# Optimization experiments

Measured on AMD Instinct MI355X. Metric: run time of the kernel, lower is better.

Reference implementation:

```python
import jax, jax.numpy as jnp
import numpy as np


def setup_inputs() -> dict:
    key = jax.random.key(0)
    x = jax.random.normal(key, (1024, 65536), dtype=jnp.float32)
    return {"input": x}


def reference(input) -> jnp.ndarray:
    B = input.shape[0]
    flat = input.reshape(B, -1)            # [B, N]
    N = flat.shape[1]
    idx = int(N * 0.8)                      # 80th-percentile position (ascending sort)
    cutoff = jnp.sort(flat, axis=-1)[:, idx]  # [B]
    cutoff = jax.lax.stop_gradient(cutoff)
    # broadcast cutoff back over all non-batch dims
    cutoff = cutoff.reshape((B,) + (1,) * (input.ndim - 1))
    return jax.nn.relu(input - cutoff)
```

## Files before the change

kernel.cpp:

```cpp
#include <hip/hip_runtime.h>


#define TPB   512
#define F4PT  32
#define NB    2048
#define CAP   6144
#define TINY  64
#define BLO   0.72f
#define BHI   0.98f

__device__ __forceinline__ unsigned f2ord(float f) {
    unsigned u = __float_as_uint(f);
    return (u & 0x80000000u) ? ~u : (u | 0x80000000u);
}
__device__ __forceinline__ float ord2f(unsigned u) {
    unsigned b = (u & 0x80000000u) ? (u ^ 0x80000000u) : ~u;
    return __uint_as_float(b);
}

__device__ __forceinline__ void hist_select(const unsigned* hist, unsigned r, int tid,
                                            unsigned* wsum, unsigned* wbase,
                                            int* s_bin, unsigned* s_cum) {
    const int lane = tid & 63, wid = tid >> 6;
    const int b0 = tid * (NB / TPB);
    unsigned h0 = hist[b0], h1 = hist[b0+1], h2 = hist[b0+2], h3 = hist[b0+3];
    unsigned s = h0 + h1 + h2 + h3;
    unsigned incl = s;
    #pragma unroll
    for (int off = 1; off < 64; off <<= 1) {
        unsigned t = __shfl_up(incl, off);
        if (lane >= off) incl += t;
    }
    if (lane == 63) wsum[wid] = incl;
    __syncthreads();
    if (tid == 0) {
        unsigned c = 0;
        #pragma unroll
        for (int w = 0; w < TPB/64; ++w) { wbase[w] = c; c += wsum[w]; }
    }
    __syncthreads();
    unsigned excl = wbase[wid] + incl - s;
    if (r >= excl && r < excl + s) {
        unsigned c = excl;
        if (r < c + h0)        { *s_bin = b0;     *s_cum = c; }
        else { c += h0; if (r < c + h1) { *s_bin = b0 + 1; *s_cum = c; }
        else { c += h1; if (r < c + h2) { *s_bin = b0 + 2; *s_cum = c; }
        else { c += h2;                   *s_bin = b0 + 3; *s_cum = c; } } }
    }
    __syncthreads();
}

__global__ __launch_bounds__(TPB)
void xsrelu_fused(const float* __restrict__ in, float* __restrict__ out,
                  int N, int k) {
    const int row  = blockIdx.x;
    const int tid  = threadIdx.x;
    const int lane = tid & 63;
    const float SCALE = (float)NB / (BHI - BLO);
    const float4* __restrict__ rowv = (const float4*)(in + (size_t)row * (size_t)N);
    float4* __restrict__ outv = (float4*)(out + (size_t)row * (size_t)N);

    __shared__ unsigned hist[NB];
    __shared__ unsigned cand[CAP];
    __shared__ unsigned tiny[TINY];
    __shared__ unsigned wsum[TPB/64], wbase[TPB/64];
    __shared__ unsigned s_cnt, s_below, s_cum, s_tc;
    __shared__ int s_bin, s_fb;
    __shared__ float s_cut;

    for (int i = tid; i < NB; i += TPB) hist[i] = 0u;
    if (tid == 0) { s_cnt = 0u; s_below = 0u; s_tc = 0u; s_fb = 0; }
    __syncthreads();

    float4 v[F4PT];
    #pragma unroll
    for (int j = 0; j < F4PT; ++j) v[j] = rowv[tid + j * TPB];

    unsigned below = 0;
    #pragma unroll
    for (int j = 0; j < F4PT; ++j) {
        const float f0 = v[j].x, f1 = v[j].y, f2 = v[j].z, f3 = v[j].w;
        below += (f0 < BLO) ? 1u : 0u;
        below += (f1 < BLO) ? 1u : 0u;
        below += (f2 < BLO) ? 1u : 0u;
        below += (f3 < BLO) ? 1u : 0u;
        if (f0 >= BLO && f0 < BHI) { unsigned p = atomicAdd(&s_cnt, 1u); if (p < CAP) cand[p] = __float_as_uint(f0); }
        if (f1 >= BLO && f1 < BHI) { unsigned p = atomicAdd(&s_cnt, 1u); if (p < CAP) cand[p] = __float_as_uint(f1); }
        if (f2 >= BLO && f2 < BHI) { unsigned p = atomicAdd(&s_cnt, 1u); if (p < CAP) cand[p] = __float_as_uint(f2); }
        if (f3 >= BLO && f3 < BHI) { unsigned p = atomicAdd(&s_cnt, 1u); if (p < CAP) cand[p] = __float_as_uint(f3); }
    }
    #pragma unroll
    for (int o = 32; o > 0; o >>= 1) below += __shfl_down(below, o);
    if (lane == 0) atomicAdd(&s_below, below);
    __syncthreads();

    const unsigned M0 = s_cnt;
    const long long r2ll = (long long)k - (long long)s_below;
    const bool fast = (M0 <= CAP) && (r2ll >= 0) && (r2ll < (long long)M0);

    if (fast) {
        const unsigned r2 = (unsigned)r2ll;
        for (unsigned i = tid; i < M0; i += TPB) {
            float f = __uint_as_float(cand[i]);
            int b = (int)((f - BLO) * SCALE);
            b = b < 0 ? 0 : (b >= NB ? NB - 1 : b);
            atomicAdd(&hist[b], 1u);
        }
        __syncthreads();
        hist_select(hist, r2, tid, wsum, wbase, &s_bin, &s_cum);
        const int bin = s_bin;
        const unsigned r3 = r2 - s_cum;
        for (unsigned i = tid; i < M0; i += TPB) {
            unsigned u = cand[i];
            float f = __uint_as_float(u);
            int b = (int)((f - BLO) * SCALE);
            b = b < 0 ? 0 : (b >= NB ? NB - 1 : b);
            if (b == bin) { unsigned p = atomicAdd(&s_tc, 1u); if (p < TINY) tiny[p] = u; }
        }
        __syncthreads();
        const unsigned c = s_tc;
        if (c > TINY) { if (tid == 0) s_fb = 1; }
        else if (tid < 64) {
            unsigned uj = (lane < (int)c) ? tiny[lane] : 0xFFFFFFFFu;
            unsigned less = 0, eq = 0;
            for (unsigned i2 = 0; i2 < c; ++i2) {
                unsigned ui = tiny[i2];
                less += (ui < uj) ? 1u : 0u;
                eq   += (ui == uj) ? 1u : 0u;
            }
            bool cond = (lane < (int)c) && (less <= r3) && (r3 < less + eq);
            unsigned long long cm = __ballot(cond);
            if (cond && lane == __ffsll((long long)cm) - 1)
                s_cut = __uint_as_float(uj);
        }
    } else {
        if (tid == 0) s_fb = 1;
    }
    __syncthreads();

    if (s_fb) {
        unsigned prefix = 0;
        unsigned rr = (unsigned)k;
        const int shifts[3] = {21, 10, 0};
        const int bitsc[3]  = {11, 11, 10};
        for (int pass = 0; pass < 3; ++pass) {
            const int sh = shifts[pass];
            const unsigned nbm = (1u << bitsc[pass]) - 1u;
            for (int i = tid; i < NB; i += TPB) hist[i] = 0u;
            __syncthreads();
            #pragma unroll
            for (int j = 0; j < F4PT; ++j) {
                const float vals[4] = {v[j].x, v[j].y, v[j].z, v[j].w};
                #pragma unroll
                for (int q = 0; q < 4; ++q) {
                    unsigned u = f2ord(vals[q]);
                    if (pass == 0 || (u >> (sh + bitsc[pass])) == prefix)
                        atomicAdd(&hist[(u >> sh) & nbm], 1u);
                }
            }
            __syncthreads();
            hist_select(hist, rr, tid, wsum, wbase, &s_bin, &s_cum);
            prefix = (prefix << bitsc[pass]) | (unsigned)s_bin;
            rr -= s_cum;
        }
        if (tid == 0) s_cut = ord2f(prefix);
        __syncthreads();
    }

    const float cut = s_cut;

    #pragma unroll
    for (int j = 0; j < F4PT; ++j) {
        float4 o;
        o.x = fmaxf(v[j].x - cut, 0.0f);
        o.y = fmaxf(v[j].y - cut, 0.0f);
        o.z = fmaxf(v[j].z - cut, 0.0f);
        o.w = fmaxf(v[j].w - cut, 0.0f);
        outv[tid + j * TPB] = o;
    }
}

extern "C" void kernel_launch(void* const* d_in, const int* in_sizes, int n_in,
                              void* d_out, int out_size, void* d_ws, size_t ws_size,
                              hipStream_t stream) {
    const float* in = (const float*)d_in[0];
    float* out = (float*)d_out;
    const int N = 65536;
    const int B = in_sizes[0] / N;
    const int k = (int)(((long long)N * 4) / 5);

    xsrelu_fused<<<dim3(B), dim3(TPB), 0, stream>>>(in, out, N, k);
}
```

Measured before the change: 475.0 us.

## Stream row from global memory instead of holding it in registers

New measurement: 481.4 us. Within noise of the previous version (+1.3%).

```diff
diff --git a/kernel.cpp b/kernel.cpp
--- a/kernel.cpp
+++ b/kernel.cpp
@@ -1,13 +1,14 @@
 #include <hip/hip_runtime.h>
 
 
-#define TPB   512
-#define F4PT  32
+#define TPB   256
+#define BPT   8
 #define NB    2048
 #define CAP   6144
 #define TINY  64
 #define BLO   0.72f
 #define BHI   0.98f
+#define NWAVE (TPB/64)
 
 __device__ __forceinline__ unsigned f2ord(float f) {
     unsigned u = __float_as_uint(f);
@@ -17,14 +18,17 @@
     unsigned b = (u & 0x80000000u) ? (u ^ 0x80000000u) : ~u;
     return __uint_as_float(b);
 }
+__device__ __forceinline__ bool in_band(float f) { return f >= BLO && f < BHI; }
 
 __device__ __forceinline__ void hist_select(const unsigned* hist, unsigned r, int tid,
                                             unsigned* wsum, unsigned* wbase,
                                             int* s_bin, unsigned* s_cum) {
     const int lane = tid & 63, wid = tid >> 6;
-    const int b0 = tid * (NB / TPB);
-    unsigned h0 = hist[b0], h1 = hist[b0+1], h2 = hist[b0+2], h3 = hist[b0+3];
-    unsigned s = h0 + h1 + h2 + h3;
+    const int b0 = tid * BPT;
+    unsigned h[BPT];
+    unsigned s = 0;
+    #pragma unroll
+    for (int j = 0; j < BPT; ++j) { h[j] = hist[b0 + j]; s += h[j]; }
     unsigned incl = s;
     #pragma unroll
     for (int off = 1; off < 64; off <<= 1) {
@@ -36,16 +40,17 @@
     if (tid == 0) {
         unsigned c = 0;
         #pragma unroll
-        for (int w = 0; w < TPB/64; ++w) { wbase[w] = c; c += wsum[w]; }
+        for (int w = 0; w < NWAVE; ++w) { wbase[w] = c; c += wsum[w]; }
     }
     __syncthreads();
     unsigned excl = wbase[wid] + incl - s;
     if (r >= excl && r < excl + s) {
         unsigned c = excl;
-        if (r < c + h0)        { *s_bin = b0;     *s_cum = c; }
-        else { c += h0; if (r < c + h1) { *s_bin = b0 + 1; *s_cum = c; }
-        else { c += h1; if (r < c + h2) { *s_bin = b0 + 2; *s_cum = c; }
-        else { c += h2;                   *s_bin = b0 + 3; *s_cum = c; } } }
+        #pragma unroll
+        for (int j = 0; j < BPT; ++j) {
+            if (r < c + h[j]) { *s_bin = b0 + j; *s_cum = c; break; }
+            c += h[j];
+        }
     }
     __syncthreads();
 }
@@ -56,6 +61,7 @@
     const int row  = blockIdx.x;
     const int tid  = threadIdx.x;
     const int lane = tid & 63;
+    const int nv   = N >> 2;
     const float SCALE = (float)NB / (BHI - BLO);
     const float4* __restrict__ rowv = (const float4*)(in + (size_t)row * (size_t)N);
     float4* __restrict__ outv = (float4*)(out + (size_t)row * (size_t)N);
@@ -63,7 +69,7 @@
     __shared__ unsigned hist[NB];
     __shared__ unsigned cand[CAP];
     __shared__ unsigned tiny[TINY];
-    __shared__ unsigned wsum[TPB/64], wbase[TPB/64];
+    __shared__ unsigned wsum[NWAVE], wbase[NWAVE];
     __shared__ unsigned s_cnt, s_below, s_cum, s_tc;
     __shared__ int s_bin, s_fb;
     __shared__ float s_cut;
@@ -72,22 +78,18 @@
     if (tid == 0) { s_cnt = 0u; s_below = 0u; s_tc = 0u; s_fb = 0; }
     __syncthreads();
 
-    float4 v[F4PT];
-    #pragma unroll
-    for (int j = 0; j < F4PT; ++j) v[j] = rowv[tid + j * TPB];
-
     unsigned below = 0;
-    #pragma unroll
-    for (int j = 0; j < F4PT; ++j) {
-        const float f0 = v[j].x, f1 = v[j].y, f2 = v[j].z, f3 = v[j].w;
-        below += (f0 < BLO) ? 1u : 0u;
-        below += (f1 < BLO) ? 1u : 0u;
-        below += (f2 < BLO) ? 1u : 0u;
-        below += (f3 < BLO) ? 1u : 0u;
-        if (f0 >= BLO && f0 < BHI) { unsigned p = atomicAdd(&s_cnt, 1u); if (p < CAP) cand[p] = __float_as_uint(f0); }
-        if (f1 >= BLO && f1 < BHI) { unsigned p = atomicAdd(&s_cnt, 1u); if (p < CAP) cand[p] = __float_as_uint(f1); }
-        if (f2 >= BLO && f2 < BHI) { unsigned p = atomicAdd(&s_cnt, 1u); if (p < CAP) cand[p] = __float_as_uint(f2); }
-        if (f3 >= BLO && f3 < BHI) { unsigned p = atomicAdd(&s_cnt, 1u); if (p < CAP) cand[p] = __float_as_uint(f3); }
+    for (int i = tid; i < nv; i += TPB) {
+        float4 v = rowv[i];
+        const float f[4] = {v.x, v.y, v.z, v.w};
+        #pragma unroll
+        for (int q = 0; q < 4; ++q) {
+            below += (f[q] < BLO) ? 1u : 0u;
+            if (in_band(f[q])) {
+                unsigned p = atomicAdd(&s_cnt, 1u);
+                if (p < CAP) cand[p] = __float_as_uint(f[q]);
+            }
+        }
     }
     #pragma unroll
     for (int o = 32; o > 0; o >>= 1) below += __shfl_down(below, o);
@@ -115,7 +117,7 @@
             float f = __uint_as_float(u);
             int b = (int)((f - BLO) * SCALE);
             b = b < 0 ? 0 : (b >= NB ? NB - 1 : b);
-            if (b == bin) { unsigned p = atomicAdd(&s_tc, 1u); if (p < TINY) tiny[p] = u; }
+            if (b == bin) { unsigned pp = atomicAdd(&s_tc, 1u); if (pp < TINY) tiny[pp] = u; }
         }
         __syncthreads();
         const unsigned c = s_tc;
@@ -148,12 +150,12 @@
             const unsigned nbm = (1u << bitsc[pass]) - 1u;
             for (int i = tid; i < NB; i += TPB) hist[i] = 0u;
             __syncthreads();
-            #pragma unroll
-            for (int j = 0; j < F4PT; ++j) {
-                const float vals[4] = {v[j].x, v[j].y, v[j].z, v[j].w};
+            for (int i = tid; i < nv; i += TPB) {
+                float4 v = rowv[i];
+                const float f[4] = {v.x, v.y, v.z, v.w};
                 #pragma unroll
                 for (int q = 0; q < 4; ++q) {
-                    unsigned u = f2ord(vals[q]);
+                    unsigned u = f2ord(f[q]);
                     if (pass == 0 || (u >> (sh + bitsc[pass])) == prefix)
                         atomicAdd(&hist[(u >> sh) & nbm], 1u);
                 }
@@ -169,14 +171,14 @@
 
     const float cut = s_cut;
 
-    #pragma unroll
-    for (int j = 0; j < F4PT; ++j) {
+    for (int i = tid; i < nv; i += TPB) {
+        float4 v = rowv[i];
         float4 o;
-        o.x = fmaxf(v[j].x - cut, 0.0f);
-        o.y = fmaxf(v[j].y - cut, 0.0f);
-        o.z = fmaxf(v[j].z - cut, 0.0f);
-        o.w = fmaxf(v[j].w - cut, 0.0f);
-        outv[tid + j * TPB] = o;
+        o.x = fmaxf(v.x - cut, 0.0f);
+        o.y = fmaxf(v.y - cut, 0.0f);
+        o.z = fmaxf(v.z - cut, 0.0f);
+        o.w = fmaxf(v.w - cut, 0.0f);
+        outv[i] = o;
     }
 }
 
```
